# Kernel optimization log

Measured on AMD Instinct MI355X. Metric: run time of the kernel, lower is better.

## Reference

```python
import jax, jax.numpy as jnp
import numpy as np

B, S, V, D = 4, 2048, 50265, 768
H_LF, DH = 12, 64          # longformer-base heads
C, W = 256, 256            # chunk size, one-sided window
DFF = 3072
NH, DK = 4, 768            # outer MultiHeadAttention(n_head=4, d_k=d_v=768)


def layer_norm(x, g, b, eps=1e-5):
    mu = jnp.mean(x, axis=-1, keepdims=True)
    var = jnp.var(x, axis=-1, keepdims=True)
    return (x - mu) * jax.lax.rsqrt(var + eps) * g + b


def _overlap_chunks(t):
    # t: [B,H,S,dh] -> [B,H,nc,3c,dh] key blocks (chunks j-1,j,j+1, zero-padded at ends)
    nc = S // C
    tp = jnp.pad(t, ((0, 0), (0, 0), (C, C), (0, 0)))
    tr = tp.reshape(t.shape[0], t.shape[1], nc + 2, C, t.shape[-1])
    return jnp.concatenate([tr[:, :, :nc], tr[:, :, 1:nc + 1], tr[:, :, 2:]], axis=3)


def sliding_window_attn(q, k, v):
    # exact band attention: query i attends keys j with |i-j| <= W
    nc = S // C
    qc = q.reshape(q.shape[0], q.shape[1], nc, C, DH)
    kb = _overlap_chunks(k)
    vb = _overlap_chunks(v)
    scores = jnp.einsum('bhncd,bhnkd->bhnck', qc, kb) / np.sqrt(DH)
    ci = jnp.arange(C)[:, None]
    ki = jnp.arange(3 * C)[None, :]
    band = jnp.abs(ki - C - ci) <= W                      # [c,3c]
    n = jnp.arange(nc)[:, None]
    kpos = n * C - C + jnp.arange(3 * C)[None, :]
    valid = (kpos >= 0) & (kpos < S)                      # [nc,3c]
    mask = band[None, :, :] & valid[:, None, :]           # [nc,c,3c]
    scores = jnp.where(mask[None, None], scores, -1e9)
    a = jax.nn.softmax(scores, axis=-1)
    out = jnp.einsum('bhnck,bhnkd->bhncd', a, vb)
    return out.reshape(q.shape)


def longformer_layer(x, emb, pos, ln_e_g, ln_e_b, lf_wq, lf_wk, lf_wv, lf_wo,
                     ln1_g, ln1_b, w1, w2, ln2_g, ln2_b):
    h = layer_norm(emb[x] + pos[None], ln_e_g, ln_e_b)    # [B,S,D]
    def heads(w):
        return (h @ w).reshape(B, S, H_LF, DH).transpose(0, 2, 1, 3)
    q, k, v = heads(lf_wq), heads(lf_wk), heads(lf_wv)
    a = sliding_window_attn(q, k, v)                      # [B,H,S,dh]
    a = a.transpose(0, 2, 1, 3).reshape(B, S, D) @ lf_wo
    h = layer_norm(h + a, ln1_g, ln1_b)
    f = jax.nn.gelu(h @ w1) @ w2
    return layer_norm(h + f, ln2_g, ln2_b)


def mha_and_pool(x, out_lf, mha_wq, mha_wk, mha_wv, mha_fc, mha_ln_g, mha_ln_b):
    residual = out_lf
    def heads(w):
        return (out_lf @ w).reshape(B, S, NH, DK).transpose(0, 2, 1, 3)
    q, k, v = heads(mha_wq), heads(mha_wk), heads(mha_wv)
    scores = jnp.einsum('bhqd,bhkd->bhqk', q, k) / np.sqrt(DK)
    key_mask = (x != 0)[:, None, None, :]
    scores = jnp.where(key_mask, scores, -1e9)
    a = jax.nn.softmax(scores, axis=-1)
    o = jnp.einsum('bhqk,bhkd->bhqd', a, v)
    o = o.transpose(0, 2, 1, 3).reshape(B, S, NH * DK) @ mha_fc
    out_attn = layer_norm(o + residual, mha_ln_g, mha_ln_b)
    return jnp.max(out_attn, axis=1)                      # max_pool1d over seq -> [B,D]


def setup_inputs() -> dict:
    key = jax.random.key(0)
    ks = jax.random.split(key, 16)
    s = 0.02
    d = {
        'x': jax.random.randint(ks[0], (B, S), 0, V),
        'emb': jax.random.normal(ks[1], (V, D), jnp.float32) * s,
        'pos': jax.random.normal(ks[2], (S, D), jnp.float32) * s,
        'ln_e_g': jnp.ones((D,), jnp.float32), 'ln_e_b': jnp.zeros((D,), jnp.float32),
        'lf_wq': jax.random.normal(ks[3], (D, D), jnp.float32) * s,
        'lf_wk': jax.random.normal(ks[4], (D, D), jnp.float32) * s,
        'lf_wv': jax.random.normal(ks[5], (D, D), jnp.float32) * s,
        'lf_wo': jax.random.normal(ks[6], (D, D), jnp.float32) * s,
        'ln1_g': jnp.ones((D,), jnp.float32), 'ln1_b': jnp.zeros((D,), jnp.float32),
        'w1': jax.random.normal(ks[7], (D, DFF), jnp.float32) * s,
        'w2': jax.random.normal(ks[8], (DFF, D), jnp.float32) * s,
        'ln2_g': jnp.ones((D,), jnp.float32), 'ln2_b': jnp.zeros((D,), jnp.float32),
        'mha_wq': jax.random.normal(ks[9], (D, NH * DK), jnp.float32) * s,
        'mha_wk': jax.random.normal(ks[10], (D, NH * DK), jnp.float32) * s,
        'mha_wv': jax.random.normal(ks[11], (D, NH * DK), jnp.float32) * s,
        'mha_fc': jax.random.normal(ks[12], (NH * DK, D), jnp.float32) * s,
        'mha_ln_g': jnp.ones((D,), jnp.float32), 'mha_ln_b': jnp.zeros((D,), jnp.float32),
    }
    return d


def reference(x, emb, pos, ln_e_g, ln_e_b, lf_wq, lf_wk, lf_wv, lf_wo,
              ln1_g, ln1_b, w1, w2, ln2_g, ln2_b,
              mha_wq, mha_wk, mha_wv, mha_fc, mha_ln_g, mha_ln_b):
    out_lf = longformer_layer(x, emb, pos, ln_e_g, ln_e_b, lf_wq, lf_wk, lf_wv, lf_wo,
                              ln1_g, ln1_b, w1, w2, ln2_g, ln2_b)
    out_lf = jax.lax.stop_gradient(out_lf)  # torch.no_grad() around longformer
    return mha_and_pool(x, out_lf, mha_wq, mha_wk, mha_wv, mha_fc, mha_ln_g, mha_ln_b)
```

## Files before the change

kernel.cpp:

```cpp
#include <hip/hip_runtime.h>
#include <hip/hip_bf16.h>
#include <math.h>

#define DEV static __device__ __forceinline__

typedef unsigned short u16;
typedef __attribute__((ext_vector_type(8))) __bf16 bf16x8;
typedef __attribute__((ext_vector_type(8))) unsigned short u16x8;
typedef __attribute__((ext_vector_type(4))) unsigned short u16x4;
typedef __attribute__((ext_vector_type(4))) float f32x4;
typedef __attribute__((ext_vector_type(4))) int i32x4;

constexpr int SL  = 2048;
constexpr int DM  = 768;
constexpr int DH  = 64;
constexpr int DFF = 3072;
constexpr int DKM = 768;

DEV float b2f(u16 u){ union{float f; unsigned u;} c; c.u = ((unsigned)u)<<16; return c.f; }
DEV u16 f2b(float f){ union{float f; unsigned u;} c; c.f=f; unsigned r=(c.u + 0x7fffu + ((c.u>>16)&1u))>>16; return (u16)r; }

DEV void gld16(u16* lds, const u16* g){
  __builtin_amdgcn_global_load_lds((const __attribute__((address_space(1))) void*)g,
                                   (__attribute__((address_space(3))) void*)lds, 16, 0, 0);
}

DEV float wred_sum(float v){
#pragma unroll
  for (int o=32;o;o>>=1) v += __shfl_xor(v,o,64);
  return v;
}
DEV float wred_max(float v){
#pragma unroll
  for (int o=32;o;o>>=1) v = fmaxf(v, __shfl_xor(v,o,64));
  return v;
}
DEV float bred_sum(float v, float* sm){
  v = wred_sum(v);
  if ((threadIdx.x & 63)==0) sm[threadIdx.x>>6] = v;
  __syncthreads();
  float r = sm[0]+sm[1]+sm[2]+sm[3];
  __syncthreads();
  return r;
}

#define PHASE_SYNC \
  __builtin_amdgcn_s_barrier(); \
  asm volatile("s_waitcnt lgkmcnt(0)" ::: "memory"); \
  __builtin_amdgcn_sched_barrier(0); \
  __builtin_amdgcn_s_setprio(1);
#define PHASE_END \
  __builtin_amdgcn_s_setprio(0); \
  __builtin_amdgcn_s_barrier();

#define MFMA_PH(MH, NH) \
  { _Pragma("unroll") for (int mi2=0; mi2<4; ++mi2) { \
      _Pragma("unroll") for (int ni2=0; ni2<2; ++ni2) { \
        acc[(MH)*4+mi2][(NH)*2+ni2] = __builtin_amdgcn_mfma_f32_16x16x32_bf16(Af[mi2][0], Bf[(NH)*2+ni2][0], acc[(MH)*4+mi2][(NH)*2+ni2], 0,0,0); \
        acc[(MH)*4+mi2][(NH)*2+ni2] = __builtin_amdgcn_mfma_f32_16x16x32_bf16(Af[mi2][1], Bf[(NH)*2+ni2][1], acc[(MH)*4+mi2][(NH)*2+ni2], 0,0,0); } } }

template<int MODE, int EPI>
__global__ __launch_bounds__(512,2) void gemm256_k(
    const u16* __restrict__ A, const u16* __restrict__ Bt,
    float* __restrict__ Cf, u16* __restrict__ Cb,
    u16* __restrict__ Cb2, u16* __restrict__ Cb3,
    int K, int lda, int ldb, int ldc)
{
  extern __shared__ u16 lds_dyn[];
  const int tid = threadIdx.x, lane = tid & 63, wv = tid >> 6;
  const int wr = wv >> 2, wc = wv & 3;
  int bx = blockIdx.x, by = blockIdx.y;
  if constexpr (MODE==0 || MODE==3) {
    const int gy = gridDim.y;
    const int k8 = bx & 7, j = (bx >> 3) + 4*by;
    bx = k8*4 + j/gy;  by = j - (j/gy)*gy;
  }
  const int m0 = bx * 256, n0 = by * 256, z = blockIdx.z;
  const int nt = K >> 6;

  int bb = 0, hh = 0;
  long long baseA = 0, baseB = 0;
  if constexpr (MODE==1) { bb=z>>2; hh=z&3; baseA=(long long)bb*SL*3072 + hh*DKM; baseB=baseA; }

  const int rb = (wv*64 + lane) >> 3;
  const int sg = ((lane & 7) ^ (rb & 7)) * 8;
  const int rd0 = (lane & 15)*64 + (((lane>>4) ^ (lane & 7)) * 8);
  const int rd1 = rd0 ^ 32;

  auto stageA = [&](int buf, int half, int kt) {
#pragma unroll
    for (int tt = 0; tt < 2; ++tt) {
      const int t = half + tt*2;
      gld16(lds_dyn + buf*16384 + t*4096 + wv*512,
            A + baseA + (long long)(m0 + t*64 + rb)*lda + (long long)kt*64 + sg);
    }
  };
  auto stageB = [&](int buf, int half, int kt) {
#pragma unroll
    for (int tt = 0; tt < 2; ++tt) {
      const int t = half*2 + tt;
      gld16(lds_dyn + 32768 + buf*16384 + t*4096 + wv*512,
            Bt + baseB + (long long)(n0 + t*64 + rb)*ldb + (long long)kt*64 + sg);
    }
  };

  f32x4 acc[8][4] = {};
  bf16x8 Af[4][2];
  bf16x8 Bf[4][2];

  stageA(0,0,0); stageB(0,0,0); stageB(0,1,0); stageA(0,1,0);
  stageA(1,0,1); stageB(1,0,1); stageB(1,1,1);
  asm volatile("s_waitcnt vmcnt(6)" ::: "memory");
  __builtin_amdgcn_s_barrier();

  for (int t = 0; t < nt; ++t) {
    const int d = t & 1;
    const u16* As_d = lds_dyn + d*16384;
    const u16* Bs_d = lds_dyn + 32768 + d*16384;
#pragma unroll
    for (int mi2=0; mi2<4; ++mi2) {
      const u16* p = As_d + (wr*128 + mi2*16)*64;
      Af[mi2][0] = *(const bf16x8*)(p + rd0);
      Af[mi2][1] = *(const bf16x8*)(p + rd1);
    }
#pragma unroll
    for (int ni2=0; ni2<2; ++ni2) {
      const u16* p = Bs_d + (wc*64 + ni2*16)*64;
      Bf[ni2][0] = *(const bf16x8*)(p + rd0);
      Bf[ni2][1] = *(const bf16x8*)(p + rd1);
    }
    if (t+1 < nt) stageA(d^1, 1, t+1);
    PHASE_SYNC; MFMA_PH(0,0); PHASE_END;
#pragma unroll
    for (int ni2=0; ni2<2; ++ni2) {
      const u16* p = Bs_d + (wc*64 + 32 + ni2*16)*64;
      Bf[2+ni2][0] = *(const bf16x8*)(p + rd0);
      Bf[2+ni2][1] = *(const bf16x8*)(p + rd1);
    }
    if (t+2 < nt) stageA(d, 0, t+2);
    PHASE_SYNC; MFMA_PH(0,1); PHASE_END;
#pragma unroll
    for (int mi2=0; mi2<4; ++mi2) {
      const u16* p = As_d + (wr*128 + 64 + mi2*16)*64;
      Af[mi2][0] = *(const bf16x8*)(p + rd0);
      Af[mi2][1] = *(const bf16x8*)(p + rd1);
    }
    if (t+2 < nt) stageB(d, 0, t+2);
    PHASE_SYNC; MFMA_PH(1,0); PHASE_END;
    if (t+2 < nt) stageB(d, 1, t+2);
    __builtin_amdgcn_s_barrier();
    __builtin_amdgcn_s_setprio(1);
    MFMA_PH(1,1);
    __builtin_amdgcn_s_setprio(0);
    if (t+2 < nt)      { asm volatile("s_waitcnt vmcnt(6)" ::: "memory"); }
    else if (t+1 < nt) { asm volatile("s_waitcnt vmcnt(0)" ::: "memory"); }
    __builtin_amdgcn_s_barrier();
  }

#pragma unroll
  for (int mi=0; mi<8; ++mi)
#pragma unroll
  for (int ni=0; ni<4; ++ni)
#pragma unroll
  for (int r=0; r<4; ++r) {
    int m = m0 + wr*128 + mi*16 + ((lane>>4)<<2) + r;
    int n = n0 + wc*64  + ni*16 + (lane & 15);
    float v = acc[mi][ni][r];
    if constexpr (EPI==2) {
      float u = 0.7978845608f*(v + 0.044715f*v*v*v);
      float th = 1.f - 2.f/(__expf(2.f*u)+1.f);
      v = 0.5f*v*(1.f + th);
    }
    if constexpr (EPI==3) v *= 0.0360843918f;
    if constexpr (MODE==3) {
      int seg = n / 3072, nn = n - seg*3072;
      u16* dst = seg==0 ? Cb : (seg==1 ? Cb2 : Cb3);
      dst[(long long)m*3072 + nn] = f2b(v);
    } else {
      long long ci;
      if constexpr (MODE==1) ci = (long long)z*SL*SL + (long long)m*SL + n;
      else                   ci = (long long)m*ldc + n;
      if constexpr (EPI==0) Cf[ci] = v; else Cb[ci] = f2b(v);
    }
  }
}

#define MFMA_Q(MB, NB, AF) \
  { _Pragma("unroll") for (int mi2=0; mi2<2; ++mi2) { \
      _Pragma("unroll") for (int ni2=0; ni2<2; ++ni2) { \
        acc[(MB)+mi2][(NB)+ni2] = __builtin_amdgcn_mfma_f32_16x16x32_bf16(AF[mi2][0], Bf[(NB)+ni2][0], acc[(MB)+mi2][(NB)+ni2], 0,0,0); \
        acc[(MB)+mi2][(NB)+ni2] = __builtin_amdgcn_mfma_f32_16x16x32_bf16(AF[mi2][1], Bf[(NB)+ni2][1], acc[(MB)+mi2][(NB)+ni2], 0,0,0); } } }

__global__ __launch_bounds__(512,2) void gemm128n_k(
    const u16* __restrict__ A, const u16* __restrict__ Bt, u16* __restrict__ Cb, int K)
{
  extern __shared__ u16 lds_dyn[];
  const int tid = threadIdx.x, lane = tid & 63, wv = tid >> 6;
  const int wr = wv >> 1, wc = wv & 1;
  const int m0 = blockIdx.x * 256, n0 = blockIdx.y * 128, z = blockIdx.z;
  const int bb = z >> 2, hh = z & 3;
  const long long baseA = (long long)z*SL*SL;
  const long long baseB = ((long long)bb*3072 + hh*DKM)*SL;
  const int nt = K >> 6;

  const int rb = (wv*64 + lane) >> 3;
  const int sg = ((lane & 7) ^ (rb & 7)) * 8;
  const int rd0 = (lane & 15)*64 + (((lane>>4) ^ (lane & 7)) * 8);
  const int rd1 = rd0 ^ 32;

  auto stageA = [&](int buf, int half, int kt) {
#pragma unroll
    for (int tt = 0; tt < 2; ++tt) {
      const int t = half*2 + tt;
      gld16(lds_dyn + buf*16384 + t*4096 + wv*512,
            A + baseA + (long long)(m0 + t*64 + rb)*SL + (long long)kt*64 + sg);
    }
  };
  auto stageB = [&](int buf, int idx, int kt) {
    gld16(lds_dyn + 32768 + buf*8192 + idx*4096 + wv*512,
          Bt + baseB + (long long)(n0 + idx*64 + rb)*SL + (long long)kt*64 + sg);
  };

  f32x4 acc[4][4] = {};
  bf16x8 Af[2][2];
  bf16x8 Bf[4][2];

  stageA(0,0,0); stageB(0,0,0); stageB(0,1,0); stageA(0,1,0);
  stageA(1,0,1); stageB(1,0,1); stageB(1,1,1);
  asm volatile("s_waitcnt vmcnt(4)" ::: "memory");
  __builtin_amdgcn_s_barrier();

  for (int t = 0; t < nt; ++t) {
    const int d = t & 1;
    const u16* As_d = lds_dyn + d*16384;
    const u16* Bs_d = lds_dyn + 32768 + d*8192;
#pragma unroll
    for (int mi2=0; mi2<2; ++mi2) {
      const u16* p = As_d + (wr*32 + mi2*16)*64;
      Af[mi2][0] = *(const bf16x8*)(p + rd0);
      Af[mi2][1] = *(const bf16x8*)(p + rd1);
    }
#pragma unroll
    for (int ni2=0; ni2<2; ++ni2) {
      const u16* p = Bs_d + (wc*64 + ni2*16)*64;
      Bf[ni2][0] = *(const bf16x8*)(p + rd0);
      Bf[ni2][1] = *(const bf16x8*)(p + rd1);
    }
    if (t+1 < nt) stageA(d^1, 1, t+1);
    PHASE_SYNC; MFMA_Q(0,0,Af); PHASE_END;
#pragma unroll
    for (int ni2=0; ni2<2; ++ni2) {
      const u16* p = Bs_d + (wc*64 + 32 + ni2*16)*64;
      Bf[2+ni2][0] = *(const bf16x8*)(p + rd0);
      Bf[2+ni2][1] = *(const bf16x8*)(p + rd1);
    }
    if (t+2 < nt) stageA(d, 0, t+2);
    PHASE_SYNC; MFMA_Q(0,2,Af); PHASE_END;
#pragma unroll
    for (int mi2=0; mi2<2; ++mi2) {
      const u16* p = As_d + (128 + wr*32 + mi2*16)*64;
      Af[mi2][0] = *(const bf16x8*)(p + rd0);
      Af[mi2][1] = *(const bf16x8*)(p + rd1);
    }
    if (t+2 < nt) stageB(d, 0, t+2);
    PHASE_SYNC; MFMA_Q(2,0,Af); PHASE_END;
    if (t+2 < nt) stageB(d, 1, t+2);
    __builtin_amdgcn_s_barrier();
    __builtin_amdgcn_s_setprio(1);
    MFMA_Q(2,2,Af);
    __builtin_amdgcn_s_setprio(0);
    if (t+2 < nt)      { asm volatile("s_waitcnt vmcnt(4)" ::: "memory"); }
    else if (t+1 < nt) { asm volatile("s_waitcnt vmcnt(0)" ::: "memory"); }
    __builtin_amdgcn_s_barrier();
  }

#pragma unroll
  for (int mi=0; mi<4; ++mi)
#pragma unroll
  for (int ni=0; ni<4; ++ni)
#pragma unroll
  for (int r=0; r<4; ++r) {
    int m = m0 + (mi>>1)*128 + wr*32 + (mi&1)*16 + ((lane>>4)<<2) + r;
    int n = n0 + wc*64 + ni*16 + (lane & 15);
    Cb[((long long)bb*SL + m)*3072 + hh*DKM + n] = f2b(acc[mi][ni][r]);
  }
}

template<int BM, int BN, int MODE, int EPI>
__global__ __launch_bounds__(256) void gemm_k(
    const u16* __restrict__ A, const u16* __restrict__ Bt,
    float* __restrict__ Cf, u16* __restrict__ Cb,
    u16* __restrict__ Cb2, u16* __restrict__ Cb3,
    int K, int lda, int ldb, int ldc)
{
  constexpr int BK = 32;
  constexpr int WM = BM/2, WN = BN/2, FM = WM/16, FN = WN/16;
  __shared__ __attribute__((aligned(16))) u16 As[BM*BK];
  __shared__ __attribute__((aligned(16))) u16 Bs[BN*BK];
  const int tid = threadIdx.x, lane = tid & 63, wv = tid >> 6;
  const int wr = wv >> 1, wc = wv & 1;
  const int m0 = blockIdx.x * BM, n0 = blockIdx.y * BN;

  f32x4 acc[FM][FN] = {};

  for (int kt = 0; kt < K; kt += BK) {
#pragma unroll
    for (int t = 0; t < (BM*4)/256; ++t) {
      int cb  = (t*4 + wv)*64;
      int ch  = cb + lane;
      int row = ch >> 2, cp = ch & 3;
      int gp  = cp ^ (row & 3) ^ ((row >> 2) & 1);
      long long ga = (long long)(m0 + row)*lda + (kt + gp*8);
      gld16(&As[cb*8], A + ga);
    }
#pragma unroll
    for (int t = 0; t < (BN*4)/256; ++t) {
      int cb  = (t*4 + wv)*64;
      int ch  = cb + lane;
      int row = ch >> 2, cp = ch & 3;
      int gp  = cp ^ (row & 3) ^ ((row >> 2) & 1);
      long long gb = (long long)(n0 + row)*ldb + (kt + gp*8);
      gld16(&Bs[cb*8], Bt + gb);
    }
    __syncthreads();
    bf16x8 af[FM], bfr[FN];
#pragma unroll
    for (int mi=0; mi<FM; ++mi) {
      int row = wr*WM + mi*16 + (lane & 15);
      int cp  = (lane >> 4) ^ (row & 3) ^ ((row >> 2) & 1);
      af[mi] = *reinterpret_cast<const bf16x8*>(&As[row*BK + cp*8]);
    }
#pragma unroll
    for (int ni=0; ni<FN; ++ni) {
      int row = wc*WN + ni*16 + (lane & 15);
      int cp  = (lane >> 4) ^ (row & 3) ^ ((row >> 2) & 1);
      bfr[ni] = *reinterpret_cast<const bf16x8*>(&Bs[row*BK + cp*8]);
    }
#pragma unroll
    for (int mi=0; mi<FM; ++mi)
#pragma unroll
      for (int ni=0; ni<FN; ++ni)
        acc[mi][ni] = __builtin_amdgcn_mfma_f32_16x16x32_bf16(af[mi], bfr[ni], acc[mi][ni], 0,0,0);
    __syncthreads();
  }

#pragma unroll
  for (int mi=0; mi<FM; ++mi)
#pragma unroll
  for (int ni=0; ni<FN; ++ni)
#pragma unroll
  for (int r=0; r<4; ++r) {
    int m = m0 + wr*WM + mi*16 + ((lane>>4)<<2) + r;
    int n = n0 + wc*WN + ni*16 + (lane & 15);
    float v = acc[mi][ni][r];
    if constexpr (MODE==5) {
      int seg = n / 768, nn = n - seg*768;
      u16* dst = seg==0 ? Cb : (seg==1 ? Cb2 : Cb3);
      dst[(long long)m*768 + nn] = f2b(v);
    } else {
      long long ci = (long long)m*ldc + n;
      if constexpr (EPI==0) Cf[ci] = v; else Cb[ci] = f2b(v);
    }
  }
}

__global__ __launch_bounds__(256) void sw_attn_k(
    const u16* __restrict__ Qm, const u16* __restrict__ Km,
    const u16* __restrict__ Vt, u16* __restrict__ Om)
{
  __shared__ __attribute__((aligned(16))) u16 Kb_s[64*64];
  __shared__ __attribute__((aligned(16))) u16 Vb_s[64*64];
  __shared__ __attribute__((aligned(16))) u16 Pb_s[4*32*64];
  const int tid = threadIdx.x, lane = tid & 63, wv = tid >> 6;
  const int qc = blockIdx.x >> 1, half = blockIdx.x & 1;
  const int h = blockIdx.y, b = blockIdx.z;
  const int q0 = qc*256 + half*128 + wv*32;
  const long long rowbase = (long long)b*SL;

  bf16x8 Qf[2][2];
#pragma unroll
  for (int mi=0;mi<2;++mi)
#pragma unroll
    for (int ks=0;ks<2;++ks)
      Qf[mi][ks] = *(const bf16x8*)(Qm + (rowbase + q0 + mi*16 + (lane&15))*DM + h*DH + ks*32 + (lane>>4)*8);

  f32x4 accO[2][4] = {};
  float mrun[2][4], lrun[2][4];
#pragma unroll
  for (int mi=0;mi<2;++mi)
#pragma unroll
    for (int r=0;r<4;++r){ mrun[mi][r]=-3e38f; lrun[mi][r]=0.f; }

  const int srow = tid >> 3;
  const int schunk = (tid & 7) ^ (srow & 7);

  const int kb0 = qc*256 + half*128 - 256;
  const int slo = kb0 < 0 ? ((-kb0) >> 6) : 0;
  const int shi_t = (SL - kb0) >> 6;
  const int shi = shi_t < 10 ? shi_t : 10;

  const int qpb = q0 + ((lane>>4)<<2);

  for (int s = slo; s < shi; ++s) {
    const int kb = kb0 + s*64;
#pragma unroll
    for (int ii=0; ii<2; ++ii) {
      gld16(Kb_s + ii*2048 + wv*512,
            Km + (rowbase + kb + srow + ii*32)*DM + h*DH + schunk*8);
      gld16(Vb_s + ii*2048 + wv*512,
            Vt + ((long long)b*DM + h*DH + srow + ii*32)*SL + kb + schunk*8);
    }
    asm volatile("s_waitcnt vmcnt(0)" ::: "memory");
    __syncthreads();

    f32x4 accS[2][4] = {};
    {
      bf16x8 Kf[4][2];
#pragma unroll
      for (int nf=0;nf<4;++nf){
        int row = nf*16 + (lane&15);
#pragma unroll
        for (int ks=0;ks<2;++ks){
          int ch = ((lane>>4) + ks*4) ^ (row&7);
          Kf[nf][ks] = *(const bf16x8*)(Kb_s + row*64 + ch*8);
        }
      }
#pragma unroll
      for (int mi=0;mi<2;++mi)
#pragma unroll
        for (int nf=0;nf<4;++nf){
          accS[mi][nf] = __builtin_amdgcn_mfma_f32_16x16x32_bf16(Qf[mi][0], Kf[nf][0], accS[mi][nf], 0,0,0);
          accS[mi][nf] = __builtin_amdgcn_mfma_f32_16x16x32_bf16(Qf[mi][1], Kf[nf][1], accS[mi][nf], 0,0,0);
        }
    }

    float smax[2][4];
#pragma unroll
    for (int mi=0;mi<2;++mi)
#pragma unroll
      for (int r=0;r<4;++r) smax[mi][r] = -3e38f;
#pragma unroll
    for (int mi=0;mi<2;++mi)
#pragma unroll
      for (int nf=0;nf<4;++nf)
#pragma unroll
        for (int r=0;r<4;++r){
          int dd = (kb + nf*16 + (lane&15)) - (qpb + mi*16 + r);
          bool ok = (dd <= 256) && (dd >= -256);
          float v = ok ? accS[mi][nf][r]*0.125f : -3e38f;
          accS[mi][nf][r] = v;
          smax[mi][r] = fmaxf(smax[mi][r], v);
        }
#pragma unroll
    for (int mi=0;mi<2;++mi)
#pragma unroll
      for (int r=0;r<4;++r){
        float v = smax[mi][r];
        v = fmaxf(v, __shfl_xor(v,1,64)); v = fmaxf(v, __shfl_xor(v,2,64));
        v = fmaxf(v, __shfl_xor(v,4,64)); v = fmaxf(v, __shfl_xor(v,8,64));
        smax[mi][r] = v;
      }

#pragma unroll
    for (int mi=0;mi<2;++mi)
#pragma unroll
      for (int r=0;r<4;++r){
        float mn = fmaxf(mrun[mi][r], smax[mi][r]);
        float sc = __expf(mrun[mi][r] - mn);
        float ls = 0.f;
#pragma unroll
        for (int nf=0;nf<4;++nf){
          float sv = accS[mi][nf][r];
          float p = (sv > -1e37f) ? __expf(sv - mn) : 0.f;
          accS[mi][nf][r] = p;
          ls += p;
        }
        ls += __shfl_xor(ls,1,64); ls += __shfl_xor(ls,2,64);
        ls += __shfl_xor(ls,4,64); ls += __shfl_xor(ls,8,64);
        lrun[mi][r] = lrun[mi][r]*sc + ls;
        mrun[mi][r] = mn;
#pragma unroll
        for (int df=0;df<4;++df) accO[mi][df][r] *= sc;
      }
#pragma unroll
    for (int mi=0;mi<2;++mi)
#pragma unroll
      for (int nf=0;nf<4;++nf)
#pragma unroll
        for (int r=0;r<4;++r){
          int ql = mi*16 + ((lane>>4)<<2) + r;
          int k  = nf*16 + (lane&15);
          int ch = (k>>3) ^ (ql&7);
          Pb_s[wv*2048 + ql*64 + ch*8 + (k&7)] = f2b(accS[mi][nf][r]);
        }
    asm volatile("s_waitcnt lgkmcnt(0)" ::: "memory");
    __builtin_amdgcn_sched_barrier(0);

    {
      bf16x8 Pf[2][2], Vf[4][2];
#pragma unroll
      for (int mi=0;mi<2;++mi){
        int ql = mi*16 + (lane&15);
#pragma unroll
        for (int ks=0;ks<2;++ks){
          int ch = ((lane>>4) + ks*4) ^ (ql&7);
          Pf[mi][ks] = *(const bf16x8*)(Pb_s + wv*2048 + ql*64 + ch*8);
        }
      }
#pragma unroll
      for (int df=0;df<4;++df){
        int dr = df*16 + (lane&15);
#pragma unroll
        for (int ks=0;ks<2;++ks){
          int ch = ((lane>>4) + ks*4) ^ (dr&7);
          Vf[df][ks] = *(const bf16x8*)(Vb_s + dr*64 + ch*8);
        }
      }
#pragma unroll
      for (int mi=0;mi<2;++mi)
#pragma unroll
        for (int df=0;df<4;++df){
          accO[mi][df] = __builtin_amdgcn_mfma_f32_16x16x32_bf16(Pf[mi][0], Vf[df][0], accO[mi][df], 0,0,0);
          accO[mi][df] = __builtin_amdgcn_mfma_f32_16x16x32_bf16(Pf[mi][1], Vf[df][1], accO[mi][df], 0,0,0);
        }
    }
    __syncthreads();
  }

#pragma unroll
  for (int mi=0;mi<2;++mi)
#pragma unroll
    for (int df=0;df<4;++df)
#pragma unroll
      for (int r=0;r<4;++r){
        long long row = rowbase + qpb + mi*16 + r;
        int col = h*DH + df*16 + (lane&15);
        Om[row*DM + col] = f2b(accO[mi][df][r] / lrun[mi][r]);
      }
}

__global__ __launch_bounds__(256) void embed_ln_k(const int* __restrict__ x,
    const float* __restrict__ emb, const float* __restrict__ pos,
    const float* __restrict__ g, const float* __restrict__ bta,
    float* __restrict__ of, u16* __restrict__ ob)
{
  __shared__ float sm[4];
  const int row = blockIdx.x, s = row & (SL-1);
  const long long tok = x[row];
  const float* e = emb + tok*DM;
  const float* p = pos + (long long)s*DM;
  float v[3], su=0.f, sq=0.f;
#pragma unroll
  for (int i=0;i<3;++i){ int d=threadIdx.x+i*256; v[i]=e[d]+p[d]; su+=v[i]; sq+=v[i]*v[i]; }
  su = bred_sum(su, sm); sq = bred_sum(sq, sm);
  float mean = su*(1.f/DM), var = sq*(1.f/DM)-mean*mean, rs = rsqrtf(var+1e-5f);
#pragma unroll
  for (int i=0;i<3;++i){ int d=threadIdx.x+i*256;
    float o = (v[i]-mean)*rs*g[d] + bta[d];
    of[(long long)row*DM+d]=o; ob[(long long)row*DM+d]=f2b(o); }
}

__global__ __launch_bounds__(256) void resid_ln_k(const float* __restrict__ a, const float* __restrict__ c,
    const float* __restrict__ g, const float* __restrict__ bta,
    float* __restrict__ of, u16* __restrict__ ob)
{
  __shared__ float sm[4];
  const long long row = blockIdx.x;
  const float* ra = a + row*DM;
  const float* rc = c + row*DM;
  float v[3], su=0.f, sq=0.f;
#pragma unroll
  for (int i=0;i<3;++i){
    int d=threadIdx.x+i*256;
    v[i]=ra[d]+rc[d];
    su+=v[i]; sq+=v[i]*v[i];
  }
  su = bred_sum(su, sm); sq = bred_sum(sq, sm);
  float mean = su*(1.f/DM), var = sq*(1.f/DM)-mean*mean, rs = rsqrtf(var+1e-5f);
#pragma unroll
  for (int i=0;i<3;++i){ int d=threadIdx.x+i*256;
    float o = (v[i]-mean)*rs*g[d] + bta[d];
    of[row*DM+d]=o; if (ob) ob[row*DM+d]=f2b(o); }
}

__global__ __launch_bounds__(256) void transp_w_k(const float* __restrict__ W, u16* __restrict__ Wt, int Kd, int Nd)
{
  __shared__ float t[64][65];
  int n0 = blockIdx.x*64, k0 = blockIdx.y*64;
  int lx = threadIdx.x & 15, ly = threadIdx.x >> 4;
#pragma unroll
  for (int i=0;i<4;++i){
    const float4 v = *(const float4*)(W + (long long)(k0+ly+i*16)*Nd + n0 + lx*4);
    t[ly+i*16][lx*4+0]=v.x; t[ly+i*16][lx*4+1]=v.y; t[ly+i*16][lx*4+2]=v.z; t[ly+i*16][lx*4+3]=v.w;
  }
  __syncthreads();
#pragma unroll
  for (int i=0;i<4;++i){
    int nn = ly + i*16, kk = lx*4;
    u16x4 o = { f2b(t[kk][nn]), f2b(t[kk+1][nn]), f2b(t[kk+2][nn]), f2b(t[kk+3][nn]) };
    *(u16x4*)(Wt + (long long)(n0+nn)*Kd + k0 + kk) = o;
  }
}

__global__ __launch_bounds__(256) void transp_b_k(const u16* __restrict__ in, u16* __restrict__ out, int Nc)
{
  __shared__ u16 t[32][33];
  int c0 = blockIdx.x*32, r0 = blockIdx.y*32;
  int lx = threadIdx.x & 31, ly = threadIdx.x >> 5;
#pragma unroll
  for (int i=0;i<4;++i) t[ly+i*8][lx] = in[(long long)(r0+ly+i*8)*Nc + c0+lx];
  __syncthreads();
  int b = r0 >> 11, s0 = r0 & (SL-1);
#pragma unroll
  for (int i=0;i<4;++i) out[((long long)b*Nc + c0+ly+i*8)*SL + s0+lx] = t[lx][ly+i*8];
}

__global__ __launch_bounds__(256) void mha_softmax_k(u16* __restrict__ sc, const int* __restrict__ x)
{
  const int r = blockIdx.x*4 + (threadIdx.x >> 6);
  const int lane = threadIdx.x & 63;
  const int z = r >> 11;
  const int b = z >> 2;
  u16* row = sc + (long long)z*SL*SL + (long long)(r & (SL-1))*SL;
  const int* xb = x + b*SL;
  float v[32]; float mx = -3e38f;
#pragma unroll
  for (int i=0;i<4;++i){
    const int j0 = i*512 + lane*8;
    u16x8 pv = *(const u16x8*)(row + j0);
    i32x4 xa = *(const i32x4*)(xb + j0);
    i32x4 xc = *(const i32x4*)(xb + j0 + 4);
#pragma unroll
    for (int e=0;e<8;++e){
      int xv = e<4 ? xa[e] : xc[e-4];
      float f = (xv != 0) ? b2f(pv[e]) : -3e38f;
      v[i*8+e] = f;
      mx = fmaxf(mx, f);
    }
  }
  mx = wred_max(mx);
  float s = 0.f;
#pragma unroll
  for (int i=0;i<32;++i){ v[i] = (v[i] > -1e37f) ? __expf(v[i]-mx) : 0.f; s += v[i]; }
  s = wred_sum(s);
  float inv = 1.f/s;
#pragma unroll
  for (int i=0;i<4;++i){
    u16x8 ov;
#pragma unroll
    for (int e=0;e<8;++e) ov[e] = f2b(v[i*8+e]*inv);
    *(u16x8*)(row + i*512 + lane*8) = ov;
  }
}

__global__ __launch_bounds__(256) void pool_part_k(const float* __restrict__ f, float* __restrict__ pp)
{
  int b = blockIdx.x, ch = blockIdx.y;
  float m0=-3e38f, m1=-3e38f, m2=-3e38f;
  for (int s = ch*32; s < ch*32+32; ++s){
    const float* r = f + ((long long)b*SL + s)*DM;
    m0=fmaxf(m0,r[threadIdx.x]); m1=fmaxf(m1,r[threadIdx.x+256]); m2=fmaxf(m2,r[threadIdx.x+512]);
  }
  float* o = pp + (long long)(b*64+ch)*DM;
  o[threadIdx.x]=m0; o[threadIdx.x+256]=m1; o[threadIdx.x+512]=m2;
}

__global__ __launch_bounds__(256) void pool_red_k(const float* __restrict__ pp, float* __restrict__ out)
{
  int b = blockIdx.x;
#pragma unroll
  for (int i=0;i<3;++i){
    int d = threadIdx.x + i*256;
    float m = -3e38f;
    for (int c=0;c<64;++c) m = fmaxf(m, pp[(long long)(b*64+c)*DM + d]);
    out[(long long)b*DM + d] = m;
  }
}

extern "C" void kernel_launch(void* const* d_in, const int* in_sizes, int n_in,
                              void* d_out, int out_size, void* d_ws, size_t ws_size,
                              hipStream_t stream)
{
  const int*   x      = (const int*)  d_in[0];
  const float* emb    = (const float*)d_in[1];
  const float* pos    = (const float*)d_in[2];
  const float* ln_e_g = (const float*)d_in[3];
  const float* ln_e_b = (const float*)d_in[4];
  const float* lf_wq  = (const float*)d_in[5];
  const float* lf_wk  = (const float*)d_in[6];
  const float* lf_wv  = (const float*)d_in[7];
  const float* lf_wo  = (const float*)d_in[8];
  const float* ln1_g  = (const float*)d_in[9];
  const float* ln1_b  = (const float*)d_in[10];
  const float* w1     = (const float*)d_in[11];
  const float* w2     = (const float*)d_in[12];
  const float* ln2_g  = (const float*)d_in[13];
  const float* ln2_b  = (const float*)d_in[14];
  const float* mha_wq = (const float*)d_in[15];
  const float* mha_wk = (const float*)d_in[16];
  const float* mha_wv = (const float*)d_in[17];
  const float* mha_fc = (const float*)d_in[18];
  const float* mha_ln_g = (const float*)d_in[19];
  const float* mha_ln_b = (const float*)d_in[20];

  (void)hipFuncSetAttribute((const void*)gemm256_k<0,2>, hipFuncAttributeMaxDynamicSharedMemorySize, 131072);
  (void)hipFuncSetAttribute((const void*)gemm256_k<1,3>, hipFuncAttributeMaxDynamicSharedMemorySize, 131072);
  (void)hipFuncSetAttribute((const void*)gemm256_k<3,1>, hipFuncAttributeMaxDynamicSharedMemorySize, 131072);
  (void)hipFuncSetAttribute((const void*)gemm128n_k,     hipFuncAttributeMaxDynamicSharedMemorySize, 98304);

  const long long R = 8192;
  float* F0 = (float*)d_ws;
  float* F1 = F0 + R*DM;
  float* F2 = F1 + R*DM;
  u16* B0 = (u16*)(F2 + R*DM);
  u16* B1 = B0 + R*DM;
  u16* B2 = B1 + R*DM;
  u16* B3 = B2 + R*DM;
  u16* WT = B3 + R*DM;
  u16* G1 = WT + (long long)9216*DM;
  u16* G2 = G1 + R*DFF;
  u16* G3 = G2 + R*DFF;
  u16* SC = G3 + R*DFF;
  float* PP = (float*)(SC + (long long)16*SL*SL);

  dim3 T(256), T5(512);
  const size_t SM256 = 131072, SM128 = 98304;

  embed_ln_k<<<dim3(8192), T, 0, stream>>>(x, emb, pos, ln_e_g, ln_e_b, F0, B0);

  transp_w_k<<<dim3(12,12), T, 0, stream>>>(lf_wq, WT,               DM, DM);
  transp_w_k<<<dim3(12,12), T, 0, stream>>>(lf_wk, WT + 768*768,     DM, DM);
  transp_w_k<<<dim3(12,12), T, 0, stream>>>(lf_wv, WT + 2*768*768,   DM, DM);
  gemm_k<128,128,5,1><<<dim3(64,18), T, 0, stream>>>(B0, WT, nullptr, B1, B2, SC, DM, DM, DM, 0);
  transp_b_k<<<dim3(24,256), T, 0, stream>>>(SC, B3, DM);

  sw_attn_k<<<dim3(16,12,4), T, 0, stream>>>(B1, B2, B3, B0);

  transp_w_k<<<dim3(12,12), T, 0, stream>>>(lf_wo, WT, DM, DM);
  gemm_k<128,64,0,0><<<dim3(64,12), T, 0, stream>>>(B0, WT, F1, nullptr, nullptr, nullptr, DM, DM, DM, DM);
  resid_ln_k<<<dim3(8192), T, 0, stream>>>(F0, F1, ln1_g, ln1_b, F2, B1);

  transp_w_k<<<dim3(48,12), T, 0, stream>>>(w1, WT, DM, DFF);
  gemm256_k<0,2><<<dim3(32,12,1), T5, SM256, stream>>>(B1, WT, nullptr, G1, nullptr, nullptr, DM, DM, DM, DFF);
  transp_w_k<<<dim3(12,48), T, 0, stream>>>(w2, WT, DFF, DM);
  gemm_k<128,64,0,0><<<dim3(64,12), T, 0, stream>>>(G1, WT, F1, nullptr, nullptr, nullptr, DFF, DFF, DFF, DM);
  resid_ln_k<<<dim3(8192), T, 0, stream>>>(F2, F1, ln2_g, ln2_b, F0, B2);

  transp_w_k<<<dim3(48,12), T, 0, stream>>>(mha_wq, WT,                 DM, DFF);
  transp_w_k<<<dim3(48,12), T, 0, stream>>>(mha_wk, WT + (long long)3072*768, DM, DFF);
  transp_w_k<<<dim3(48,12), T, 0, stream>>>(mha_wv, WT + (long long)6144*768, DM, DFF);
  gemm256_k<3,1><<<dim3(32,36,1), T5, SM256, stream>>>(B2, WT, nullptr, G1, G2, SC, DM, DM, DM, 0);
  transp_b_k<<<dim3(96,256), T, 0, stream>>>(SC, G3, DFF);

  gemm256_k<1,3><<<dim3(8,8,16), T5, SM256, stream>>>(G1, G2, nullptr, SC, nullptr, nullptr, DKM, 3072, 3072, 0);
  mha_softmax_k<<<dim3(8192), T, 0, stream>>>(SC, x);
  gemm128n_k<<<dim3(8,6,16), T5, SM128, stream>>>(SC, G3, G2, SL);

  transp_w_k<<<dim3(12,48), T, 0, stream>>>(mha_fc, WT, DFF, DM);
  gemm_k<128,64,0,0><<<dim3(64,12), T, 0, stream>>>(G2, WT, F1, nullptr, nullptr, nullptr, DFF, DFF, DFF, DM);
  resid_ln_k<<<dim3(8192), T, 0, stream>>>(F0, F1, mha_ln_g, mha_ln_b, F2, nullptr);

  pool_part_k<<<dim3(4,64), T, 0, stream>>>(F2, PP);
  pool_red_k<<<dim3(4), T, 0, stream>>>(PP, (float*)d_out);
}
```

Baseline: 953.3 us.

## Stage GEMM epilogues through LDS, drop tile swizzle, widen output-projection tiles

The 256-tile and 128n GEMM epilogues now write bf16 results into a swizzled LDS buffer and then emit coalesced 16-byte row stores, replacing scattered 2-byte stores. The block-index remapping used for L2 locality in modes 0 and 3 is removed. The three D=768 output GEMMs switch from 128x64 to 128x128 tiles, which halves their grid. The LDS epilogue drops the fp32 Cf path in gemm256_k and adds extra barriers, and dropping the remap may reduce cache reuse.

New measurement: 971.4 us. Within noise of the previous version (+1.9%).

```diff
diff --git a/kernel.cpp b/kernel.cpp
--- a/kernel.cpp
+++ b/kernel.cpp
@@ -69,18 +69,11 @@
   extern __shared__ u16 lds_dyn[];
   const int tid = threadIdx.x, lane = tid & 63, wv = tid >> 6;
   const int wr = wv >> 2, wc = wv & 3;
-  int bx = blockIdx.x, by = blockIdx.y;
-  if constexpr (MODE==0 || MODE==3) {
-    const int gy = gridDim.y;
-    const int k8 = bx & 7, j = (bx >> 3) + 4*by;
-    bx = k8*4 + j/gy;  by = j - (j/gy)*gy;
-  }
-  const int m0 = bx * 256, n0 = by * 256, z = blockIdx.z;
+  const int m0 = blockIdx.x * 256, n0 = blockIdx.y * 256, z = blockIdx.z;
   const int nt = K >> 6;
 
-  int bb = 0, hh = 0;
   long long baseA = 0, baseB = 0;
-  if constexpr (MODE==1) { bb=z>>2; hh=z&3; baseA=(long long)bb*SL*3072 + hh*DKM; baseB=baseA; }
+  if constexpr (MODE==1) { int bb=z>>2, hh=z&3; baseA=(long long)bb*SL*3072 + hh*DKM; baseB=baseA; }
 
   const int rb = (wv*64 + lane) >> 3;
   const int sg = ((lane & 7) ^ (rb & 7)) * 8;
@@ -157,30 +150,48 @@
     __builtin_amdgcn_s_barrier();
   }
 
-#pragma unroll
-  for (int mi=0; mi<8; ++mi)
-#pragma unroll
-  for (int ni=0; ni<4; ++ni)
-#pragma unroll
-  for (int r=0; r<4; ++r) {
-    int m = m0 + wr*128 + mi*16 + ((lane>>4)<<2) + r;
-    int n = n0 + wc*64  + ni*16 + (lane & 15);
-    float v = acc[mi][ni][r];
-    if constexpr (EPI==2) {
-      float u = 0.7978845608f*(v + 0.044715f*v*v*v);
-      float th = 1.f - 2.f/(__expf(2.f*u)+1.f);
-      v = 0.5f*v*(1.f + th);
-    }
-    if constexpr (EPI==3) v *= 0.0360843918f;
-    if constexpr (MODE==3) {
-      int seg = n / 3072, nn = n - seg*3072;
-      u16* dst = seg==0 ? Cb : (seg==1 ? Cb2 : Cb3);
-      dst[(long long)m*3072 + nn] = f2b(v);
-    } else {
-      long long ci;
-      if constexpr (MODE==1) ci = (long long)z*SL*SL + (long long)m*SL + n;
-      else                   ci = (long long)m*ldc + n;
-      if constexpr (EPI==0) Cf[ci] = v; else Cb[ci] = f2b(v);
+  {
+    constexpr int ERS = 272;
+    u16* eb = lds_dyn;
+    u16* dstb; long long rstride;
+    if constexpr (MODE==1) { dstb = Cb + (long long)z*SL*SL + (long long)m0*SL + n0; rstride = SL; }
+    else if constexpr (MODE==3) {
+      int seg = n0 / 3072;
+      u16* d0 = seg==0 ? Cb : (seg==1 ? Cb2 : Cb3);
+      dstb = d0 + (long long)m0*3072 + (n0 - seg*3072); rstride = 3072;
+    } else { dstb = Cb + (long long)m0*ldc + n0; rstride = ldc; }
+    (void)Cf;
+#pragma unroll
+    for (int hf = 0; hf < 2; ++hf) {
+      if (wr == hf) {
+#pragma unroll
+        for (int mi=0; mi<8; ++mi)
+#pragma unroll
+        for (int ni=0; ni<4; ++ni)
+#pragma unroll
+        for (int r=0; r<4; ++r) {
+          int ml = mi*16 + ((lane>>4)<<2) + r;
+          int nl = wc*64 + ni*16 + (lane & 15);
+          float v = acc[mi][ni][r];
+          if constexpr (EPI==2) {
+            float u = 0.7978845608f*(v + 0.044715f*v*v*v);
+            float th = 1.f - 2.f/(__expf(2.f*u)+1.f);
+            v = 0.5f*v*(1.f + th);
+          }
+          if constexpr (EPI==3) v *= 0.0360843918f;
+          int ch = nl >> 3, off = nl & 7;
+          eb[ml*ERS + (((ch ^ ((ml>>2)&3)))<<3) + off] = f2b(v);
+        }
+      }
+      __syncthreads();
+#pragma unroll
+      for (int j = 0; j < 8; ++j) {
+        int c = tid + (j<<9);
+        int row = c >> 5, nch = c & 31;
+        u16x8 val = *(const u16x8*)(eb + row*ERS + (((nch ^ ((row>>2)&3)))<<3));
+        *(u16x8*)(dstb + (long long)(hf*128 + row)*rstride + (nch<<3)) = val;
+      }
+      __syncthreads();
     }
   }
 }
@@ -274,15 +285,35 @@
     __builtin_amdgcn_s_barrier();
   }
 
-#pragma unroll
-  for (int mi=0; mi<4; ++mi)
-#pragma unroll
-  for (int ni=0; ni<4; ++ni)
-#pragma unroll
-  for (int r=0; r<4; ++r) {
-    int m = m0 + (mi>>1)*128 + wr*32 + (mi&1)*16 + ((lane>>4)<<2) + r;
-    int n = n0 + wc*64 + ni*16 + (lane & 15);
-    Cb[((long long)bb*SL + m)*3072 + hh*DKM + n] = f2b(acc[mi][ni][r]);
+  {
+    constexpr int ERS = 136;
+    u16* eb = lds_dyn;
+    u16* dstb = Cb + ((long long)bb*SL + m0)*3072 + hh*DKM + n0;
+#pragma unroll
+    for (int hf = 0; hf < 2; ++hf) {
+#pragma unroll
+      for (int mi2=0; mi2<2; ++mi2) {
+        const int mi = hf*2 + mi2;
+#pragma unroll
+        for (int ni=0; ni<4; ++ni)
+#pragma unroll
+        for (int r=0; r<4; ++r) {
+          int ml = wr*32 + (mi&1)*16 + ((lane>>4)<<2) + r;
+          int nl = wc*64 + ni*16 + (lane & 15);
+          int ch = nl >> 3, off = nl & 7;
+          eb[ml*ERS + (((ch ^ ((ml>>2)&3)))<<3) + off] = f2b(acc[mi][ni][r]);
+        }
+      }
+      __syncthreads();
+#pragma unroll
+      for (int j = 0; j < 4; ++j) {
+        int c = tid + (j<<9);
+        int row = c >> 4, nch = c & 15;
+        u16x8 val = *(const u16x8*)(eb + row*ERS + (((nch ^ ((row>>2)&3)))<<3));
+        *(u16x8*)(dstb + (long long)(hf*128 + row)*3072 + (nch<<3)) = val;
+      }
+      __syncthreads();
+    }
   }
 }
 
@@ -737,27 +768,27 @@
   sw_attn_k<<<dim3(16,12,4), T, 0, stream>>>(B1, B2, B3, B0);
 
   transp_w_k<<<dim3(12,12), T, 0, stream>>>(lf_wo, WT, DM, DM);
-  gemm_k<128,64,0,0><<<dim3(64,12), T, 0, stream>>>(B0, WT, F1, nullptr, nullptr, nullptr, DM, DM, DM, DM);
+  gemm_k<128,128,0,0><<<dim3(64,6), T, 0, stream>>>(B0, WT, F1, nullptr, nullptr, nullptr, DM, DM, DM, DM);
   resid_ln_k<<<dim3(8192), T, 0, stream>>>(F0, F1, ln1_g, ln1_b, F2, B1);
 
   transp_w_k<<<dim3(48,12), T, 0, stream>>>(w1, WT, DM, DFF);
   gemm256_k<0,2><<<dim3(32,12,1), T5, SM256, stream>>>(B1, WT, nullptr, G1, nullptr, nullptr, DM, DM, DM, DFF);
   transp_w_k<<<dim3(12,48), T, 0, stream>>>(w2, WT, DFF, DM);
-  gemm_k<128,64,0,0><<<dim3(64,12), T, 0, stream>>>(G1, WT, F1, nullptr, nullptr, nullptr, DFF, DFF, DFF, DM);
+  gemm_k<128,128,0,0><<<dim3(64,6), T, 0, stream>>>(G1, WT, F1, nullptr, nullptr, nullptr, DFF, DFF, DFF, DM);
   resid_ln_k<<<dim3(8192), T, 0, stream>>>(F2, F1, ln2_g, ln2_b, F0, B2);
 
   transp_w_k<<<dim3(48,12), T, 0, stream>>>(mha_wq, WT,                 DM, DFF);
   transp_w_k<<<dim3(48,12), T, 0, stream>>>(mha_wk, WT + (long long)3072*768, DM, DFF);
   transp_w_k<<<dim3(48,12), T, 0, stream>>>(mha_wv, WT + (long long)6144*768, DM, DFF);
-  gemm256_k<3,1><<<dim3(32,36,1), T5, SM256, stream>>>(B2, WT, nullptr, G1, G2, SC, DM, DM, DM, 0);
+  gemm256_k<3,1><<<dim3(32,36,1), T5, SM256, stream>>>(B2, WT, nullptr, G1, G2, SC, DM, DM, DM, 3072);
   transp_b_k<<<dim3(96,256), T, 0, stream>>>(SC, G3, DFF);
 
-  gemm256_k<1,3><<<dim3(8,8,16), T5, SM256, stream>>>(G1, G2, nullptr, SC, nullptr, nullptr, DKM, 3072, 3072, 0);
+  gemm256_k<1,3><<<dim3(8,8,16), T5, SM256, stream>>>(G1, G2, nullptr, SC, nullptr, nullptr, DKM, 3072, 3072, SL);
   mha_softmax_k<<<dim3(8192), T, 0, stream>>>(SC, x);
   gemm128n_k<<<dim3(8,6,16), T5, SM128, stream>>>(SC, G3, G2, SL);
 
   transp_w_k<<<dim3(12,48), T, 0, stream>>>(mha_fc, WT, DFF, DM);
-  gemm_k<128,64,0,0><<<dim3(64,12), T, 0, stream>>>(G2, WT, F1, nullptr, nullptr, nullptr, DFF, DFF, DFF, DM);
+  gemm_k<128,128,0,0><<<dim3(64,6), T, 0, stream>>>(G2, WT, F1, nullptr, nullptr, nullptr, DFF, DFF, DFF, DM);
   resid_ln_k<<<dim3(8192), T, 0, stream>>>(F0, F1, mha_ln_g, mha_ln_b, F2, nullptr);
 
   pool_part_k<<<dim3(4,64), T, 0, stream>>>(F2, PP);
```
